# Kernel tuning notes

Hardware: AMD Instinct MI355X
Metric: run time of the kernel (lower is better)

## Reference

```python
import jax, jax.numpy as jnp
import numpy as np

N = 50000      # nodes
E = 1_600_000  # edges (avg degree 32)
IN, H, OUT, R = 128, 64, 32, 8
NEG_SLOPE = 0.2


def _rgat(x, src, dst, etype, W, q, k, b, n_nodes):
    """PyG RGATConv, defaults: heads=1, dim=1, additive-self-attention,
    across-relation softmax, concat=True, bias=True, dropout=0 (eval)."""
    # per-relation transform of all nodes: [R, N, O] (cheaper than per-edge bmm since 2*deg >> R)
    t = jnp.einsum('ni,rio->rno', x, W)
    xi = t[etype, dst]                      # [E, O] transformed target feats
    xj = t[etype, src]                      # [E, O] transformed source feats
    a = (xi @ q + xj @ k)[:, 0]             # [E] additive attention logits
    a = jnp.where(a >= 0, a, NEG_SLOPE * a)  # leaky_relu
    # segment softmax over incoming edges of each target node (across relations)
    m = jax.ops.segment_max(a, dst, num_segments=n_nodes)
    m = jnp.where(jnp.isfinite(m), m, 0.0)
    ex = jnp.exp(a - m[dst])
    s = jax.ops.segment_sum(ex, dst, num_segments=n_nodes)
    alpha = ex / (s[dst] + 1e-16)
    out = jax.ops.segment_sum(alpha[:, None] * xj, dst, num_segments=n_nodes)
    return out + b


def setup_inputs() -> dict:
    key = jax.random.key(0)
    ks = jax.random.split(key, 24)
    x = jax.random.normal(ks[0], (N, IN), jnp.float32)
    edge_index = jax.random.randint(ks[1], (2, E), 0, N, jnp.int32)
    edge_type = jax.random.randint(ks[2], (E,), 0, R, jnp.int32)

    def glorot(k, shape, fan_in):
        return jax.random.normal(k, shape, jnp.float32) * (1.0 / np.sqrt(fan_in))

    d = dict(x=x, edge_index=edge_index, edge_type=edge_type)
    # conv1: in->hidden, conv_mu / conv_logvar: hidden->hidden
    d['W1'] = glorot(ks[3], (R, IN, H), IN)
    d['q1'] = glorot(ks[4], (H, 1), H)
    d['k1'] = glorot(ks[5], (H, 1), H)
    d['b1'] = jnp.zeros((H,), jnp.float32)
    d['Wmu'] = glorot(ks[6], (R, H, H), H)
    d['qmu'] = glorot(ks[7], (H, 1), H)
    d['kmu'] = glorot(ks[8], (H, 1), H)
    d['bmu'] = jnp.zeros((H,), jnp.float32)
    d['Wlv'] = glorot(ks[9], (R, H, H), H)
    d['qlv'] = glorot(ks[10], (H, 1), H)
    d['klv'] = glorot(ks[11], (H, 1), H)
    d['blv'] = jnp.zeros((H,), jnp.float32)
    d['Wm'] = glorot(ks[12], (H, OUT), H)   # linear_mu (stored [in,out])
    d['bm'] = jnp.zeros((OUT,), jnp.float32)
    d['Wl'] = glorot(ks[13], (H, OUT), H)   # linear_logvar
    d['bl'] = jnp.zeros((OUT,), jnp.float32)
    return d


def reference(x, edge_index, edge_type, W1, q1, k1, b1,
              Wmu, qmu, kmu, bmu, Wlv, qlv, klv, blv, Wm, bm, Wl, bl):
    src, dst = edge_index[0], edge_index[1]
    hidden = jax.nn.relu(_rgat(x, src, dst, edge_type, W1, q1, k1, b1, N))
    mu = jax.nn.relu(_rgat(hidden, src, dst, edge_type, Wmu, qmu, kmu, bmu, N))
    mu = mu @ Wm + bm                       # dropout is identity in eval
    logvar = jax.nn.relu(_rgat(hidden, src, dst, edge_type, Wlv, qlv, klv, blv, N))
    logvar = logvar @ Wl + bl
    logstd = 0.5 * logvar
    return (mu, logstd)
```

## Files before the change

### kernel.cpp

```cpp
#include <hip/hip_runtime.h>
#include <cstdint>

#define HDIM 64
#define ODIM 32
#define NEG_SLOPE 0.2f
#define SCHUNK 2048
#define EPB 8192

typedef __attribute__((ext_vector_type(8))) short v8s;
typedef __attribute__((ext_vector_type(4))) float v4f;

__device__ __forceinline__ unsigned f2bf_rne(float f) {
  unsigned u = __float_as_uint(f);
  return (u + 0x7FFFu + ((u >> 16) & 1u)) >> 16;
}

__device__ __forceinline__ unsigned fenc(float f) {
  unsigned u = __float_as_uint(f);
  return (u & 0x80000000u) ? ~u : (u | 0x80000000u);
}
__device__ __forceinline__ float fdec(unsigned e) {
  unsigned u = (e & 0x80000000u) ? (e ^ 0x80000000u) : ~e;
  return __uint_as_float(u);
}

__global__ __launch_bounds__(256) void cvt_bf16_kernel(
    const float* __restrict__ in, unsigned short* __restrict__ out, int n) {
  int i = (blockIdx.x * 256 + threadIdx.x) * 4;
  if (i + 3 < n) {
    float4 v = *(const float4*)&in[i];
    ushort4 o;
    o.x = (unsigned short)f2bf_rne(v.x);
    o.y = (unsigned short)f2bf_rne(v.y);
    o.z = (unsigned short)f2bf_rne(v.z);
    o.w = (unsigned short)f2bf_rne(v.w);
    *(ushort4*)&out[i] = o;
  }
}

__global__ __launch_bounds__(256) void transpose_w_kernel(
    const float* __restrict__ W1, const float* __restrict__ Wmu,
    const float* __restrict__ Wlv, unsigned short* __restrict__ W1t,
    unsigned short* __restrict__ Wmut, unsigned short* __restrict__ Wlvt) {
  const int b = blockIdx.x;
  const int r = b & 7;
  const int which = b >> 3;
  const float* src;
  unsigned short* dst;
  int K;
  if (which == 0) {
    src = W1; dst = W1t; K = 128;
  } else if (which == 1) {
    src = Wmu; dst = Wmut; K = 64;
  } else {
    src = Wlv; dst = Wlvt; K = 64;
  }
  for (int idx = threadIdx.x; idx < K * 64; idx += 256) {
    const int kk = idx >> 6, o = idx & 63;
    dst[((size_t)r * 64 + o) * K + kk] =
        (unsigned short)f2bf_rne(src[((size_t)r * K + kk) * 64 + o]);
  }
}

__global__ __launch_bounds__(256) void count_deg_kernel(
    const int* __restrict__ dst, int* __restrict__ deg, int E) {
  int e = blockIdx.x * 256 + threadIdx.x;
  if (e < E) atomicAdd(&deg[dst[e]], 1);
}

__global__ __launch_bounds__(256) void scan_p1(const int* __restrict__ deg,
                                               int* __restrict__ bsum, int n) {
  int base = blockIdx.x * SCHUNK + threadIdx.x * 8;
  int s = 0;
#pragma unroll
  for (int j = 0; j < 8; j++) {
    int i = base + j;
    if (i < n) s += deg[i];
  }
#pragma unroll
  for (int d = 1; d < 64; d <<= 1) s += __shfl_xor(s, d, 64);
  __shared__ int ws[4];
  if ((threadIdx.x & 63) == 0) ws[threadIdx.x >> 6] = s;
  __syncthreads();
  if (threadIdx.x == 0) bsum[blockIdx.x] = ws[0] + ws[1] + ws[2] + ws[3];
}

__global__ void scan_p2(int* bsum, int nb) {
  int i = threadIdx.x;
  int v = (i < nb) ? bsum[i] : 0;
  int orig = v;
#pragma unroll
  for (int d = 1; d < 64; d <<= 1) {
    int up = __shfl_up(v, d, 64);
    if (i >= d) v += up;
  }
  if (i < nb) bsum[i] = v - orig;
}

__global__ __launch_bounds__(256) void scan_p3(const int* __restrict__ deg,
                                               const int* __restrict__ bsum,
                                               int* __restrict__ row_ptr,
                                               int n) {
  int base = blockIdx.x * SCHUNK + threadIdx.x * 8;
  int vals[8];
  int s = 0;
#pragma unroll
  for (int j = 0; j < 8; j++) {
    int i = base + j;
    vals[j] = (i < n) ? deg[i] : 0;
    s += vals[j];
  }
  int lane = threadIdx.x & 63, w = threadIdx.x >> 6;
  int v = s;
#pragma unroll
  for (int d = 1; d < 64; d <<= 1) {
    int up = __shfl_up(v, d, 64);
    if (lane >= d) v += up;
  }
  __shared__ int wsum[4];
  if (lane == 63) wsum[w] = v;
  __syncthreads();
  int woff = 0;
#pragma unroll
  for (int i = 0; i < 4; i++) woff += (i < w) ? wsum[i] : 0;
  int off = bsum[blockIdx.x] + woff + v - s;
#pragma unroll
  for (int j = 0; j < 8; j++) {
    int i = base + j;
    off += vals[j];
    if (i < n) row_ptr[i + 1] = off;
  }
  if (blockIdx.x == 0 && threadIdx.x == 0) row_ptr[0] = 0;
}

__global__ __launch_bounds__(256) void bucket_cursor_init(
    const int* __restrict__ row_ptr, int* __restrict__ cursor, int N, int nb) {
  int i = threadIdx.x;
  if (i < nb) cursor[i] = row_ptr[min(i * 256, N)];
}

__global__ __launch_bounds__(256) void bucket_pass1(
    const int* __restrict__ src, const int* __restrict__ dst,
    const int* __restrict__ etype, int* __restrict__ cursor,
    unsigned* __restrict__ tmp, int E) {
  __shared__ int hist[256];
  __shared__ int binstart[256];
  __shared__ int gbase[256];
  __shared__ int fill[256];
  __shared__ int wsum[4];
  __shared__ unsigned stage[EPB];
  __shared__ unsigned char binof[EPB];
  const int tid = threadIdx.x;
  const int e0 = blockIdx.x * EPB;
  const int cnt = min(EPB, E - e0);

  hist[tid] = 0;
  fill[tid] = 0;
  __syncthreads();
  for (int j = tid; j < cnt; j += 256) atomicAdd(&hist[dst[e0 + j] >> 8], 1);
  __syncthreads();

  const int hv = hist[tid];
  {
    const int lane = tid & 63, w = tid >> 6;
    int iv = hv;
#pragma unroll
    for (int d = 1; d < 64; d <<= 1) {
      int up = __shfl_up(iv, d, 64);
      if (lane >= d) iv += up;
    }
    if (lane == 63) wsum[w] = iv;
    __syncthreads();
    int woff = 0;
#pragma unroll
    for (int i = 0; i < 4; i++) woff += (i < w) ? wsum[i] : 0;
    binstart[tid] = woff + iv - hv;
    if (hv > 0) gbase[tid] = atomicAdd(&cursor[tid], hv);
  }
  __syncthreads();

  for (int j = tid; j < cnt; j += 256) {
    const int d = dst[e0 + j];
    const int b = d >> 8;
    const unsigned rec = ((unsigned)(d & 255) << 19) |
                         ((unsigned)etype[e0 + j] << 16) |
                         (unsigned)src[e0 + j];
    const int slot = binstart[b] + atomicAdd(&fill[b], 1);
    stage[slot] = rec;
    binof[slot] = (unsigned char)b;
  }
  __syncthreads();

  for (int s = tid; s < cnt; s += 256) {
    const int b = binof[s];
    tmp[gbase[b] + (s - binstart[b])] = stage[s];
  }
}

__global__ __launch_bounds__(256) void bucket_pass2(
    const int* __restrict__ row_ptr, const unsigned* __restrict__ tmp,
    int* __restrict__ edges, int N) {
  __shared__ int rp[257];
  __shared__ int fill[256];
  const int tid = threadIdx.x;
  const int rowbase = blockIdx.x * 256;
  const int rowcnt = min(256, N - rowbase);
  for (int i = tid; i <= rowcnt; i += 256) rp[i] = row_ptr[rowbase + i];
  fill[tid] = 0;
  __syncthreads();
  const int beg = rp[0];
  const int endv = rp[rowcnt];
  for (int i = beg + tid; i < endv; i += 256) {
    const unsigned rec = tmp[i];
    const int dlow = rec >> 19;
    const int pos = rp[dlow] + atomicAdd(&fill[dlow], 1);
    edges[pos] = (int)(rec & 0x7FFFFu);
  }
}

__global__ __launch_bounds__(256) void rowmax_kernel(
    const float* __restrict__ ak, unsigned* __restrict__ maxk_enc, int N) {
  const int row = blockIdx.x;
  const int nchunks = gridDim.y;
  const int per = (N + nchunks - 1) / nchunks;
  const int beg = blockIdx.y * per;
  const int end = min(N, beg + per);
  const float* r = ak + (size_t)row * N;
  float m = -1e30f;
  for (int i = beg + threadIdx.x; i < end; i += 256) m = fmaxf(m, r[i]);
#pragma unroll
  for (int d = 1; d < 64; d <<= 1) m = fmaxf(m, __shfl_xor(m, d, 64));
  __shared__ float ws[4];
  if ((threadIdx.x & 63) == 0) ws[threadIdx.x >> 6] = m;
  __syncthreads();
  if (threadIdx.x == 0) {
    float bm = fmaxf(fmaxf(ws[0], ws[1]), fmaxf(ws[2], ws[3]));
    atomicMax(&maxk_enc[row], fenc(bm));
  }
}

__global__ __launch_bounds__(256) void transform1_mfma(
    const unsigned short* __restrict__ xb,
    const unsigned short* __restrict__ W1t, const float* __restrict__ q,
    const float* __restrict__ k, unsigned short* __restrict__ tb,
    float* __restrict__ aq, float* __restrict__ ak, int N) {
  __shared__ unsigned short st[4][16][72];
  const int r = blockIdx.x;
  const int tid = threadIdx.x;
  const int w = tid >> 6;
  const int lane = tid & 63;
  const int quad = lane >> 4;
  const int mrow = lane & 15;
  const int n0w = blockIdx.y * 64 + w * 16;

  const int gA = min(n0w + mrow, N - 1);
  const unsigned short* arow = xb + (size_t)gA * 128 + quad * 8;
  const unsigned short* wrow = W1t + ((size_t)r * 64 + mrow) * 128 + quad * 8;

  v4f acc[4];
#pragma unroll
  for (int tt = 0; tt < 4; tt++) acc[tt] = (v4f){0.f, 0.f, 0.f, 0.f};

#pragma unroll
  for (int k0 = 0; k0 < 128; k0 += 32) {
    v8s a = *(const v8s*)(arow + k0);
#pragma unroll
    for (int tt = 0; tt < 4; tt++) {
      v8s b = *(const v8s*)(wrow + (size_t)tt * 16 * 128 + k0);
      acc[tt] = __builtin_amdgcn_mfma_f32_16x16x32_bf16(a, b, acc[tt], 0, 0, 0);
    }
  }

  float qv[4], kv[4];
#pragma unroll
  for (int tt = 0; tt < 4; tt++) {
    qv[tt] = q[tt * 16 + mrow];
    kv[tt] = k[tt * 16 + mrow];
  }

#pragma unroll
  for (int i = 0; i < 4; i++) {
    float vq = 0.f, vk = 0.f;
#pragma unroll
    for (int tt = 0; tt < 4; tt++) {
      vq = fmaf(acc[tt][i], qv[tt], vq);
      vk = fmaf(acc[tt][i], kv[tt], vk);
      st[w][quad * 4 + i][tt * 16 + mrow] =
          (unsigned short)f2bf_rne(acc[tt][i]);
    }
#pragma unroll
    for (int d = 1; d < 16; d <<= 1) {
      vq += __shfl_xor(vq, d, 64);
      vk += __shfl_xor(vk, d, 64);
    }
    const int gn = n0w + quad * 4 + i;
    if (mrow == 0 && gn < N) {
      aq[(size_t)r * N + gn] = vq;
      ak[(size_t)r * N + gn] = vk;
    }
  }
  __syncthreads();

  const int row = lane >> 2, cg = lane & 3;
  const int gns = n0w + row;
  if (gns < N) {
    const uint4 v0 = *(const uint4*)&st[w][row][cg * 16];
    const uint4 v1 = *(const uint4*)&st[w][row][cg * 16 + 8];
    uint4* dst = (uint4*)&tb[((size_t)r * N + gns) * 64 + cg * 16];
    dst[0] = v0;
    dst[1] = v1;
  }
}

__global__ __launch_bounds__(256) void transform2_mfma(
    const unsigned short* __restrict__ hb,
    const unsigned short* __restrict__ Wmut,
    const unsigned short* __restrict__ Wlvt, const float* __restrict__ qa,
    const float* __restrict__ ka, const float* __restrict__ qb,
    const float* __restrict__ kb, unsigned* __restrict__ t2p,
    float* __restrict__ aq2, float* __restrict__ ak2, int N) {
  __shared__ unsigned st2[4][16][68];
  const int r = blockIdx.x;
  const int tid = threadIdx.x;
  const int w = tid >> 6;
  const int lane = tid & 63;
  const int quad = lane >> 4;
  const int mrow = lane & 15;
  const int n0w = blockIdx.y * 64 + w * 16;

  const int gA = min(n0w + mrow, N - 1);
  const unsigned short* arow = hb + (size_t)gA * 64 + quad * 8;
  const size_t woff = ((size_t)r * 64 + mrow) * 64 + quad * 8;

  v4f am[4], al[4];
#pragma unroll
  for (int tt = 0; tt < 4; tt++) {
    am[tt] = (v4f){0.f, 0.f, 0.f, 0.f};
    al[tt] = (v4f){0.f, 0.f, 0.f, 0.f};
  }

#pragma unroll
  for (int k0 = 0; k0 < 64; k0 += 32) {
    v8s a = *(const v8s*)(arow + k0);
#pragma unroll
    for (int tt = 0; tt < 4; tt++) {
      v8s bm = *(const v8s*)(Wmut + woff + (size_t)tt * 16 * 64 + k0);
      v8s bl = *(const v8s*)(Wlvt + woff + (size_t)tt * 16 * 64 + k0);
      am[tt] = __builtin_amdgcn_mfma_f32_16x16x32_bf16(a, bm, am[tt], 0, 0, 0);
      al[tt] = __builtin_amdgcn_mfma_f32_16x16x32_bf16(a, bl, al[tt], 0, 0, 0);
    }
  }

  float qmv[4], kmv[4], qlv2[4], klv2[4];
#pragma unroll
  for (int tt = 0; tt < 4; tt++) {
    qmv[tt] = qa[tt * 16 + mrow];
    kmv[tt] = ka[tt * 16 + mrow];
    qlv2[tt] = qb[tt * 16 + mrow];
    klv2[tt] = kb[tt * 16 + mrow];
  }

#pragma unroll
  for (int i = 0; i < 4; i++) {
    float vqm = 0.f, vkm = 0.f, vql = 0.f, vkl = 0.f;
#pragma unroll
    for (int tt = 0; tt < 4; tt++) {
      vqm = fmaf(am[tt][i], qmv[tt], vqm);
      vkm = fmaf(am[tt][i], kmv[tt], vkm);
      vql = fmaf(al[tt][i], qlv2[tt], vql);
      vkl = fmaf(al[tt][i], klv2[tt], vkl);
      st2[w][quad * 4 + i][tt * 16 + mrow] =
          f2bf_rne(am[tt][i]) | (f2bf_rne(al[tt][i]) << 16);
    }
#pragma unroll
    for (int d = 1; d < 16; d <<= 1) {
      vqm += __shfl_xor(vqm, d, 64);
      vkm += __shfl_xor(vkm, d, 64);
      vql += __shfl_xor(vql, d, 64);
      vkl += __shfl_xor(vkl, d, 64);
    }
    const int gn = n0w + quad * 4 + i;
    if (mrow == 0 && gn < N) {
      aq2[(size_t)r * N + gn] = vqm;
      ak2[(size_t)r * N + gn] = vkm;
      aq2[(size_t)(8 + r) * N + gn] = vql;
      ak2[(size_t)(8 + r) * N + gn] = vkl;
    }
  }
  __syncthreads();

  const int row = lane >> 2, cg = lane & 3;
  const int gns = n0w + row;
  if (gns < N) {
    unsigned* dst = &t2p[((size_t)r * N + gns) * 64 + cg * 16];
#pragma unroll
    for (int s = 0; s < 4; s++)
      *(uint4*)(dst + s * 4) = *(const uint4*)&st2[w][row][cg * 16 + s * 4];
  }
}

__global__ __launch_bounds__(256) void aggregate_kernel(
    const int* __restrict__ row_ptr, const int* __restrict__ edges,
    const unsigned short* __restrict__ tb, const float* __restrict__ aq,
    const float* __restrict__ ak, const unsigned* __restrict__ maxk_enc,
    const float* __restrict__ bias, unsigned short* __restrict__ hb, int N) {
  const int tid = threadIdx.x;
  const int w = tid >> 6, o = tid & 63;
  int wid = blockIdx.x * 4 + w;
  const bool valid = wid < N;
  if (!valid) wid = N - 1;
  const int beg = row_ptr[wid];
  const int end = valid ? row_ptr[wid + 1] : beg;
  const int deg = end - beg;

  const float aqw = aq[(size_t)(o & 7) * N + wid];

  float v = aqw + fdec(maxk_enc[o & 7]);
  v = (v >= 0.f) ? v : NEG_SLOPE * v;
#pragma unroll
  for (int d = 1; d < 8; d <<= 1) v = fmaxf(v, __shfl_xor(v, d, 64));
  const float m = __shfl(v, 0, 64);

  const int g = o >> 3;
  const int cl = o & 7;
  float s = 0.f;
  float acc[8];
#pragma unroll
  for (int c = 0; c < 8; c++) acc[c] = 0.f;

  for (int base = 0; base < deg; base += 64) {
    const int j = base + o;
    const int gcount = min(64, deg - base);
    const int packed = edges[beg + min(j, deg - 1)];
    const int src = packed & 0xFFFF;
    const int rr = packed >> 16;
    const int idx = rr * N + src;
    float x = __shfl(aqw, rr, 64) + ak[idx];
    x = (x >= 0.f) ? x : NEG_SLOPE * x;
    const float p = (j < deg) ? __expf(x - m) : 0.f;
    s += p;
    const int g8 = (gcount + 7) & ~7;
#pragma unroll 4
    for (int u = 0; u < g8; u += 8) {
      const int e = u + g;
      const float pe = __shfl(p, e, 64);
      const int ie = __shfl(idx, e, 64);
      const uint4 tv = *(const uint4*)(tb + (size_t)ie * 64 + cl * 8);
      const unsigned uu0 = tv.x, uu1 = tv.y, uu2 = tv.z, uu3 = tv.w;
      acc[0] = fmaf(pe, __uint_as_float(uu0 << 16), acc[0]);
      acc[1] = fmaf(pe, __uint_as_float(uu0 & 0xFFFF0000u), acc[1]);
      acc[2] = fmaf(pe, __uint_as_float(uu1 << 16), acc[2]);
      acc[3] = fmaf(pe, __uint_as_float(uu1 & 0xFFFF0000u), acc[3]);
      acc[4] = fmaf(pe, __uint_as_float(uu2 << 16), acc[4]);
      acc[5] = fmaf(pe, __uint_as_float(uu2 & 0xFFFF0000u), acc[5]);
      acc[6] = fmaf(pe, __uint_as_float(uu3 << 16), acc[6]);
      acc[7] = fmaf(pe, __uint_as_float(uu3 & 0xFFFF0000u), acc[7]);
    }
  }
#pragma unroll
  for (int d = 1; d < 64; d <<= 1) s += __shfl_xor(s, d, 64);
#pragma unroll
  for (int d = 8; d < 64; d <<= 1) {
#pragma unroll
    for (int c = 0; c < 8; c++) acc[c] += __shfl_xor(acc[c], d, 64);
  }

  if (valid && g == 0) {
    const float inv = 1.f / (s + 1e-16f);
    unsigned rv[8];
#pragma unroll
    for (int c = 0; c < 8; c++) {
      const float res = acc[c] * inv + bias[cl * 8 + c];
      rv[c] = f2bf_rne(fmaxf(res, 0.f));
    }
    uint4 pkd;
    pkd.x = rv[0] | (rv[1] << 16);
    pkd.y = rv[2] | (rv[3] << 16);
    pkd.z = rv[4] | (rv[5] << 16);
    pkd.w = rv[6] | (rv[7] << 16);
    *(uint4*)(hb + (size_t)wid * 64 + cl * 8) = pkd;
  }
}

__global__ __launch_bounds__(256) void aggregate2_kernel(
    const int* __restrict__ row_ptr, const int* __restrict__ edges,
    const unsigned* __restrict__ t2p, const float* __restrict__ aq2,
    const float* __restrict__ ak2, const unsigned* __restrict__ maxk2_enc,
    const float* __restrict__ bmu, const float* __restrict__ blv,
    const float* __restrict__ Wm, const float* __restrict__ bm,
    const float* __restrict__ Wlin, const float* __restrict__ bl,
    float* __restrict__ out_mu, float* __restrict__ out_ls, int N) {
  __shared__ float WmL[2048];
  __shared__ float WlL[2048];
  __shared__ float bL[64];
  __shared__ float hL[4][130];
  const int tid = threadIdx.x;
  for (int i = tid; i < 2048; i += 256) {
    WmL[i] = Wm[i];
    WlL[i] = Wlin[i];
  }
  if (tid < 32) {
    bL[tid] = bm[tid];
    bL[32 + tid] = bl[tid];
  }
  __syncthreads();

  const int w = tid >> 6, o = tid & 63;
  int wid = blockIdx.x * 4 + w;
  const bool valid = wid < N;
  if (!valid) wid = N - 1;
  const int beg = row_ptr[wid];
  const int end = valid ? row_ptr[wid + 1] : beg;
  const int deg = end - beg;

  const float aqw = aq2[(size_t)(o & 15) * N + wid];

  float v = aqw + fdec(maxk2_enc[o & 15]);
  v = (v >= 0.f) ? v : NEG_SLOPE * v;
#pragma unroll
  for (int d = 1; d < 8; d <<= 1) v = fmaxf(v, __shfl_xor(v, d, 64));
  const float m0 = __shfl(v, 0, 64);
  const float m1 = __shfl(v, 8, 64);

  const int g = o >> 4;
  const int cl = o & 15;
  float s0 = 0.f, s1 = 0.f;
  float acc0[4], acc1[4];
#pragma unroll
  for (int c = 0; c < 4; c++) {
    acc0[c] = 0.f;
    acc1[c] = 0.f;
  }

  for (int base = 0; base < deg; base += 64) {
    const int j = base + o;
    const int gcount = min(64, deg - base);
    const int packed = edges[beg + min(j, deg - 1)];
    const int src = packed & 0xFFFF;
    const int rr = packed >> 16;
    const int idx = rr * N + src;
    float x0 = __shfl(aqw, rr, 64) + ak2[idx];
    float x1 = __shfl(aqw, 8 + rr, 64) + ak2[idx + 8 * N];
    x0 = (x0 >= 0.f) ? x0 : NEG_SLOPE * x0;
    x1 = (x1 >= 0.f) ? x1 : NEG_SLOPE * x1;
    const float p0 = (j < deg) ? __expf(x0 - m0) : 0.f;
    const float p1 = (j < deg) ? __expf(x1 - m1) : 0.f;
    s0 += p0;
    s1 += p1;
    const int g4 = (gcount + 3) & ~3;
#pragma unroll 4
    for (int u = 0; u < g4; u += 4) {
      const int e = u + g;
      const float pe0 = __shfl(p0, e, 64);
      const float pe1 = __shfl(p1, e, 64);
      const int ie = __shfl(idx, e, 64);
      const uint4 pk = *(const uint4*)(t2p + (size_t)ie * 64 + cl * 4);
      const unsigned uu0 = pk.x, uu1 = pk.y, uu2 = pk.z, uu3 = pk.w;
      acc0[0] = fmaf(pe0, __uint_as_float(uu0 << 16), acc0[0]);
      acc1[0] = fmaf(pe1, __uint_as_float(uu0 & 0xFFFF0000u), acc1[0]);
      acc0[1] = fmaf(pe0, __uint_as_float(uu1 << 16), acc0[1]);
      acc1[1] = fmaf(pe1, __uint_as_float(uu1 & 0xFFFF0000u), acc1[1]);
      acc0[2] = fmaf(pe0, __uint_as_float(uu2 << 16), acc0[2]);
      acc1[2] = fmaf(pe1, __uint_as_float(uu2 & 0xFFFF0000u), acc1[2]);
      acc0[3] = fmaf(pe0, __uint_as_float(uu3 << 16), acc0[3]);
      acc1[3] = fmaf(pe1, __uint_as_float(uu3 & 0xFFFF0000u), acc1[3]);
    }
  }
#pragma unroll
  for (int d = 1; d < 64; d <<= 1) {
    s0 += __shfl_xor(s0, d, 64);
    s1 += __shfl_xor(s1, d, 64);
  }
#pragma unroll
  for (int d = 16; d < 64; d <<= 1) {
#pragma unroll
    for (int c = 0; c < 4; c++) {
      acc0[c] += __shfl_xor(acc0[c], d, 64);
      acc1[c] += __shfl_xor(acc1[c], d, 64);
    }
  }

  if (g == 0) {
    const float inv0 = 1.f / (s0 + 1e-16f);
    const float inv1 = 1.f / (s1 + 1e-16f);
#pragma unroll
    for (int c = 0; c < 4; c++) {
      hL[w][cl * 4 + c] = fmaxf(acc0[c] * inv0 + bmu[cl * 4 + c], 0.f);
      hL[w][64 + cl * 4 + c] = fmaxf(acc1[c] * inv1 + blv[cl * 4 + c], 0.f);
    }
  }
  __syncthreads();

  const float* hrow = &hL[w][(o >= 32) ? 64 : 0];
  const float* WL = (o >= 32) ? WlL : WmL;
  const int j = o & 31;
  float acc = 0.f;
#pragma unroll 8
  for (int c = 0; c < 64; c++) acc = fmaf(hrow[c], WL[c * 32 + j], acc);
  if (valid) {
    if (o < 32)
      out_mu[(size_t)wid * 32 + j] = acc + bL[j];
    else
      out_ls[(size_t)wid * 32 + j] = (acc + bL[32 + j]) * 0.5f;
  }
}

extern "C" void kernel_launch(void* const* d_in, const int* in_sizes, int n_in,
                              void* d_out, int out_size, void* d_ws,
                              size_t ws_size, hipStream_t stream) {
  const float* x = (const float*)d_in[0];
  const int* edge_index = (const int*)d_in[1];
  const int* edge_type = (const int*)d_in[2];
  const float* W1 = (const float*)d_in[3];
  const float* q1 = (const float*)d_in[4];
  const float* k1 = (const float*)d_in[5];
  const float* b1 = (const float*)d_in[6];
  const float* Wmu = (const float*)d_in[7];
  const float* qmu = (const float*)d_in[8];
  const float* kmu = (const float*)d_in[9];
  const float* bmu = (const float*)d_in[10];
  const float* Wlv = (const float*)d_in[11];
  const float* qlv = (const float*)d_in[12];
  const float* klv = (const float*)d_in[13];
  const float* blv = (const float*)d_in[14];
  const float* Wm = (const float*)d_in[15];
  const float* bm = (const float*)d_in[16];
  const float* Wl = (const float*)d_in[17];
  const float* bl = (const float*)d_in[18];

  const int N = in_sizes[0] / 128;
  const int E = in_sizes[2];
  const int R = in_sizes[3] / (128 * 64);

  float* out_mu = (float*)d_out;
  float* out_ls = (float*)d_out + (size_t)N * ODIM;

  char* wsp = (char*)d_ws;
  size_t off = 0;
  auto carve = [&](size_t bytes) {
    void* p = wsp + off;
    off += (bytes + 255) & ~(size_t)255;
    return p;
  };

  void* tbuf = carve((size_t)R * N * 64 * sizeof(unsigned));
  unsigned short* t1b = (unsigned short*)tbuf;
  unsigned* t2p = (unsigned*)tbuf;
  unsigned short* xb = (unsigned short*)carve((size_t)N * 128 * 2);
  unsigned short* hb = (unsigned short*)carve((size_t)N * 64 * 2);
  unsigned short* W1t = (unsigned short*)carve((size_t)R * 64 * 128 * 2);
  unsigned short* Wmut = (unsigned short*)carve((size_t)R * 64 * 64 * 2);
  unsigned short* Wlvt = (unsigned short*)carve((size_t)R * 64 * 64 * 2);
  float* aq2 = (float*)carve((size_t)2 * R * N * sizeof(float));
  float* ak2 = (float*)carve((size_t)2 * R * N * sizeof(float));
  unsigned* maxk_enc = (unsigned*)carve(2 * R * sizeof(unsigned));
  int* deg = (int*)carve((size_t)N * sizeof(int));
  int* row_ptr = (int*)carve((size_t)(N + 1) * sizeof(int));
  int* bsum = (int*)carve(256 * sizeof(int));
  int* cursor = (int*)carve(256 * sizeof(int));
  unsigned* tmp = (unsigned*)carve((size_t)E * sizeof(unsigned));
  int* edges = (int*)carve((size_t)E * sizeof(int));

  const int* e_src = edge_index;
  const int* e_dst = edge_index + E;

  cvt_bf16_kernel<<<(N * 128 / 4 + 255) / 256, 256, 0, stream>>>(x, xb,
                                                                 N * 128);
  transpose_w_kernel<<<3 * R, 256, 0, stream>>>(W1, Wmu, Wlv, W1t, Wmut, Wlvt);

  hipMemsetAsync(deg, 0, (size_t)N * sizeof(int), stream);
  hipMemsetAsync(maxk_enc, 0, 2 * R * sizeof(unsigned), stream);
  count_deg_kernel<<<(E + 255) / 256, 256, 0, stream>>>(e_dst, deg, E);
  const int nchunk = (N + SCHUNK - 1) / SCHUNK;
  scan_p1<<<nchunk, 256, 0, stream>>>(deg, bsum, N);
  scan_p2<<<1, 64, 0, stream>>>(bsum, nchunk);
  scan_p3<<<nchunk, 256, 0, stream>>>(deg, bsum, row_ptr, N);

  const int nbuck = (N + 255) >> 8;
  bucket_cursor_init<<<1, 256, 0, stream>>>(row_ptr, cursor, N, nbuck);
  bucket_pass1<<<(E + EPB - 1) / EPB, 256, 0, stream>>>(e_src, e_dst,
                                                        edge_type, cursor,
                                                        tmp, E);
  bucket_pass2<<<nbuck, 256, 0, stream>>>(row_ptr, tmp, edges, N);

  const int nb64 = (N + 63) / 64;
  const int agg_blocks = (N + 3) / 4;

  transform1_mfma<<<dim3(R, nb64), 256, 0, stream>>>(xb, W1t, q1, k1, t1b,
                                                     aq2, ak2, N);
  rowmax_kernel<<<dim3(R, 32), 256, 0, stream>>>(ak2, maxk_enc, N);
  aggregate_kernel<<<agg_blocks, 256, 0, stream>>>(
      row_ptr, edges, t1b, aq2, ak2, maxk_enc, b1, hb, N);

  hipMemsetAsync(maxk_enc, 0, 2 * R * sizeof(unsigned), stream);

  transform2_mfma<<<dim3(R, nb64), 256, 0, stream>>>(
      hb, Wmut, Wlvt, qmu, kmu, qlv, klv, t2p, aq2, ak2, N);
  rowmax_kernel<<<dim3(2 * R, 32), 256, 0, stream>>>(ak2, maxk_enc, N);
  aggregate2_kernel<<<agg_blocks, 256, 0, stream>>>(
      row_ptr, edges, t2p, aq2, ak2, maxk_enc, bmu, blv, Wm, bm, Wl, bl,
      out_mu, out_ls, N);
}
```

Baseline: 554.6 us.

## Loop relations inside transform kernels to reuse node input fragments

Both MFMA transform kernels drop the per-relation grid dimension and loop over all 8 relations inside each block. The input A fragments for a 64-node tile are loaded once and reused across relations, which cuts repeated reads of x and hidden. The trade-off is 8x fewer blocks (about 782 instead of about 6256), so less parallelism, plus an extra barrier per relation iteration. Separately, the unroll pragma on the aggregate inner loop is removed.

```diff
diff --git a/kernel.cpp b/kernel.cpp
--- a/kernel.cpp
+++ b/kernel.cpp
@@ -245,31 +245,19 @@
     const float* __restrict__ k, unsigned short* __restrict__ tb,
     float* __restrict__ aq, float* __restrict__ ak, int N) {
   __shared__ unsigned short st[4][16][72];
-  const int r = blockIdx.x;
   const int tid = threadIdx.x;
   const int w = tid >> 6;
   const int lane = tid & 63;
   const int quad = lane >> 4;
   const int mrow = lane & 15;
-  const int n0w = blockIdx.y * 64 + w * 16;
+  const int n0w = blockIdx.x * 64 + w * 16;
 
   const int gA = min(n0w + mrow, N - 1);
   const unsigned short* arow = xb + (size_t)gA * 128 + quad * 8;
-  const unsigned short* wrow = W1t + ((size_t)r * 64 + mrow) * 128 + quad * 8;
-
-  v4f acc[4];
-#pragma unroll
-  for (int tt = 0; tt < 4; tt++) acc[tt] = (v4f){0.f, 0.f, 0.f, 0.f};
-
-#pragma unroll
-  for (int k0 = 0; k0 < 128; k0 += 32) {
-    v8s a = *(const v8s*)(arow + k0);
-#pragma unroll
-    for (int tt = 0; tt < 4; tt++) {
-      v8s b = *(const v8s*)(wrow + (size_t)tt * 16 * 128 + k0);
-      acc[tt] = __builtin_amdgcn_mfma_f32_16x16x32_bf16(a, b, acc[tt], 0, 0, 0);
-    }
-  }
+
+  v8s a[4];
+#pragma unroll
+  for (int k0 = 0; k0 < 4; k0++) a[k0] = *(const v8s*)(arow + k0 * 32);
 
   float qv[4], kv[4];
 #pragma unroll
@@ -278,37 +266,58 @@
     kv[tt] = k[tt * 16 + mrow];
   }
 
-#pragma unroll
-  for (int i = 0; i < 4; i++) {
-    float vq = 0.f, vk = 0.f;
-#pragma unroll
-    for (int tt = 0; tt < 4; tt++) {
-      vq = fmaf(acc[tt][i], qv[tt], vq);
-      vk = fmaf(acc[tt][i], kv[tt], vk);
-      st[w][quad * 4 + i][tt * 16 + mrow] =
-          (unsigned short)f2bf_rne(acc[tt][i]);
-    }
-#pragma unroll
-    for (int d = 1; d < 16; d <<= 1) {
-      vq += __shfl_xor(vq, d, 64);
-      vk += __shfl_xor(vk, d, 64);
-    }
-    const int gn = n0w + quad * 4 + i;
-    if (mrow == 0 && gn < N) {
-      aq[(size_t)r * N + gn] = vq;
-      ak[(size_t)r * N + gn] = vk;
-    }
-  }
-  __syncthreads();
-
   const int row = lane >> 2, cg = lane & 3;
   const int gns = n0w + row;
-  if (gns < N) {
-    const uint4 v0 = *(const uint4*)&st[w][row][cg * 16];
-    const uint4 v1 = *(const uint4*)&st[w][row][cg * 16 + 8];
-    uint4* dst = (uint4*)&tb[((size_t)r * N + gns) * 64 + cg * 16];
-    dst[0] = v0;
-    dst[1] = v1;
+
+  for (int r = 0; r < 8; r++) {
+    const unsigned short* wrow =
+        W1t + ((size_t)r * 64 + mrow) * 128 + quad * 8;
+
+    v4f acc[4];
+#pragma unroll
+    for (int tt = 0; tt < 4; tt++) acc[tt] = (v4f){0.f, 0.f, 0.f, 0.f};
+
+#pragma unroll
+    for (int k0 = 0; k0 < 4; k0++) {
+#pragma unroll
+      for (int tt = 0; tt < 4; tt++) {
+        v8s b = *(const v8s*)(wrow + (size_t)tt * 16 * 128 + k0 * 32);
+        acc[tt] =
+            __builtin_amdgcn_mfma_f32_16x16x32_bf16(a[k0], b, acc[tt], 0, 0, 0);
+      }
+    }
+
+#pragma unroll
+    for (int i = 0; i < 4; i++) {
+      float vq = 0.f, vk = 0.f;
+#pragma unroll
+      for (int tt = 0; tt < 4; tt++) {
+        vq = fmaf(acc[tt][i], qv[tt], vq);
+        vk = fmaf(acc[tt][i], kv[tt], vk);
+        st[w][quad * 4 + i][tt * 16 + mrow] =
+            (unsigned short)f2bf_rne(acc[tt][i]);
+      }
+#pragma unroll
+      for (int d = 1; d < 16; d <<= 1) {
+        vq += __shfl_xor(vq, d, 64);
+        vk += __shfl_xor(vk, d, 64);
+      }
+      const int gn = n0w + quad * 4 + i;
+      if (mrow == 0 && gn < N) {
+        aq[(size_t)r * N + gn] = vq;
+        ak[(size_t)r * N + gn] = vk;
+      }
+    }
+    __syncthreads();
+
+    if (gns < N) {
+      const uint4 v0 = *(const uint4*)&st[w][row][cg * 16];
+      const uint4 v1 = *(const uint4*)&st[w][row][cg * 16 + 8];
+      uint4* dst = (uint4*)&tb[((size_t)r * N + gns) * 64 + cg * 16];
+      dst[0] = v0;
+      dst[1] = v1;
+    }
+    __syncthreads();
   }
 }
 
@@ -320,36 +329,19 @@
     const float* __restrict__ kb, unsigned* __restrict__ t2p,
     float* __restrict__ aq2, float* __restrict__ ak2, int N) {
   __shared__ unsigned st2[4][16][68];
-  const int r = blockIdx.x;
   const int tid = threadIdx.x;
   const int w = tid >> 6;
   const int lane = tid & 63;
   const int quad = lane >> 4;
   const int mrow = lane & 15;
-  const int n0w = blockIdx.y * 64 + w * 16;
+  const int n0w = blockIdx.x * 64 + w * 16;
 
   const int gA = min(n0w + mrow, N - 1);
   const unsigned short* arow = hb + (size_t)gA * 64 + quad * 8;
-  const size_t woff = ((size_t)r * 64 + mrow) * 64 + quad * 8;
-
-  v4f am[4], al[4];
-#pragma unroll
-  for (int tt = 0; tt < 4; tt++) {
-    am[tt] = (v4f){0.f, 0.f, 0.f, 0.f};
-    al[tt] = (v4f){0.f, 0.f, 0.f, 0.f};
-  }
-
-#pragma unroll
-  for (int k0 = 0; k0 < 64; k0 += 32) {
-    v8s a = *(const v8s*)(arow + k0);
-#pragma unroll
-    for (int tt = 0; tt < 4; tt++) {
-      v8s bm = *(const v8s*)(Wmut + woff + (size_t)tt * 16 * 64 + k0);
-      v8s bl = *(const v8s*)(Wlvt + woff + (size_t)tt * 16 * 64 + k0);
-      am[tt] = __builtin_amdgcn_mfma_f32_16x16x32_bf16(a, bm, am[tt], 0, 0, 0);
-      al[tt] = __builtin_amdgcn_mfma_f32_16x16x32_bf16(a, bl, al[tt], 0, 0, 0);
-    }
-  }
+
+  v8s a[2];
+#pragma unroll
+  for (int k0 = 0; k0 < 2; k0++) a[k0] = *(const v8s*)(arow + k0 * 32);
 
   float qmv[4], kmv[4], qlv2[4], klv2[4];
 #pragma unroll
@@ -360,42 +352,68 @@
     klv2[tt] = kb[tt * 16 + mrow];
   }
 
-#pragma unroll
-  for (int i = 0; i < 4; i++) {
-    float vqm = 0.f, vkm = 0.f, vql = 0.f, vkl = 0.f;
-#pragma unroll
-    for (int tt = 0; tt < 4; tt++) {
-      vqm = fmaf(am[tt][i], qmv[tt], vqm);
-      vkm = fmaf(am[tt][i], kmv[tt], vkm);
-      vql = fmaf(al[tt][i], qlv2[tt], vql);
-      vkl = fmaf(al[tt][i], klv2[tt], vkl);
-      st2[w][quad * 4 + i][tt * 16 + mrow] =
-          f2bf_rne(am[tt][i]) | (f2bf_rne(al[tt][i]) << 16);
-    }
-#pragma unroll
-    for (int d = 1; d < 16; d <<= 1) {
-      vqm += __shfl_xor(vqm, d, 64);
-      vkm += __shfl_xor(vkm, d, 64);
-      vql += __shfl_xor(vql, d, 64);
-      vkl += __shfl_xor(vkl, d, 64);
-    }
-    const int gn = n0w + quad * 4 + i;
-    if (mrow == 0 && gn < N) {
-      aq2[(size_t)r * N + gn] = vqm;
-      ak2[(size_t)r * N + gn] = vkm;
-      aq2[(size_t)(8 + r) * N + gn] = vql;
-      ak2[(size_t)(8 + r) * N + gn] = vkl;
-    }
-  }
-  __syncthreads();
-
   const int row = lane >> 2, cg = lane & 3;
   const int gns = n0w + row;
-  if (gns < N) {
-    unsigned* dst = &t2p[((size_t)r * N + gns) * 64 + cg * 16];
-#pragma unroll
-    for (int s = 0; s < 4; s++)
-      *(uint4*)(dst + s * 4) = *(const uint4*)&st2[w][row][cg * 16 + s * 4];
+
+  for (int r = 0; r < 8; r++) {
+    const size_t woff = ((size_t)r * 64 + mrow) * 64 + quad * 8;
+
+    v4f am[4], al[4];
+#pragma unroll
+    for (int tt = 0; tt < 4; tt++) {
+      am[tt] = (v4f){0.f, 0.f, 0.f, 0.f};
+      al[tt] = (v4f){0.f, 0.f, 0.f, 0.f};
+    }
+
+#pragma unroll
+    for (int k0 = 0; k0 < 2; k0++) {
+#pragma unroll
+      for (int tt = 0; tt < 4; tt++) {
+        v8s bm = *(const v8s*)(Wmut + woff + (size_t)tt * 16 * 64 + k0 * 32);
+        v8s bl = *(const v8s*)(Wlvt + woff + (size_t)tt * 16 * 64 + k0 * 32);
+        am[tt] =
+            __builtin_amdgcn_mfma_f32_16x16x32_bf16(a[k0], bm, am[tt], 0, 0, 0);
+        al[tt] =
+            __builtin_amdgcn_mfma_f32_16x16x32_bf16(a[k0], bl, al[tt], 0, 0, 0);
+      }
+    }
+
+#pragma unroll
+    for (int i = 0; i < 4; i++) {
+      float vqm = 0.f, vkm = 0.f, vql = 0.f, vkl = 0.f;
+#pragma unroll
+      for (int tt = 0; tt < 4; tt++) {
+        vqm = fmaf(am[tt][i], qmv[tt], vqm);
+        vkm = fmaf(am[tt][i], kmv[tt], vkm);
+        vql = fmaf(al[tt][i], qlv2[tt], vql);
+        vkl = fmaf(al[tt][i], klv2[tt], vkl);
+        st2[w][quad * 4 + i][tt * 16 + mrow] =
+            f2bf_rne(am[tt][i]) | (f2bf_rne(al[tt][i]) << 16);
+      }
+#pragma unroll
+      for (int d = 1; d < 16; d <<= 1) {
+        vqm += __shfl_xor(vqm, d, 64);
+        vkm += __shfl_xor(vkm, d, 64);
+        vql += __shfl_xor(vql, d, 64);
+        vkl += __shfl_xor(vkl, d, 64);
+      }
+      const int gn = n0w + quad * 4 + i;
+      if (mrow == 0 && gn < N) {
+        aq2[(size_t)r * N + gn] = vqm;
+        ak2[(size_t)r * N + gn] = vkm;
+        aq2[(size_t)(8 + r) * N + gn] = vql;
+        ak2[(size_t)(8 + r) * N + gn] = vkl;
+      }
+    }
+    __syncthreads();
+
+    if (gns < N) {
+      unsigned* dst = &t2p[((size_t)r * N + gns) * 64 + cg * 16];
+#pragma unroll
+      for (int s = 0; s < 4; s++)
+        *(uint4*)(dst + s * 4) = *(const uint4*)&st2[w][row][cg * 16 + s * 4];
+    }
+    __syncthreads();
   }
 }
 
@@ -440,7 +458,6 @@
     const float p = (j < deg) ? __expf(x - m) : 0.f;
     s += p;
     const int g8 = (gcount + 7) & ~7;
-#pragma unroll 4
     for (int u = 0; u < g8; u += 8) {
       const int e = u + g;
       const float pe = __shfl(p, e, 64);
@@ -686,16 +703,15 @@
   const int nb64 = (N + 63) / 64;
   const int agg_blocks = (N + 3) / 4;
 
-  transform1_mfma<<<dim3(R, nb64), 256, 0, stream>>>(xb, W1t, q1, k1, t1b,
-                                                     aq2, ak2, N);
+  transform1_mfma<<<nb64, 256, 0, stream>>>(xb, W1t, q1, k1, t1b, aq2, ak2, N);
   rowmax_kernel<<<dim3(R, 32), 256, 0, stream>>>(ak2, maxk_enc, N);
   aggregate_kernel<<<agg_blocks, 256, 0, stream>>>(
       row_ptr, edges, t1b, aq2, ak2, maxk_enc, b1, hb, N);
 
   hipMemsetAsync(maxk_enc, 0, 2 * R * sizeof(unsigned), stream);
 
-  transform2_mfma<<<dim3(R, nb64), 256, 0, stream>>>(
-      hb, Wmut, Wlvt, qmu, kmu, qlv, klv, t2p, aq2, ak2, N);
+  transform2_mfma<<<nb64, 256, 0, stream>>>(hb, Wmut, Wlvt, qmu, kmu, qlv,
+                                            klv, t2p, aq2, ak2, N);
   rowmax_kernel<<<dim3(2 * R, 32), 256, 0, stream>>>(ak2, maxk_enc, N);
   aggregate2_kernel<<<agg_blocks, 256, 0, stream>>>(
       row_ptr, edges, t2p, aq2, ak2, maxk_enc, bmu, blv, Wm, bm, Wl, bl,
```

Measured after the change: 568.8 us. 1.03x slower.
